# Performance work log

Measured on AMD Instinct MI355X. Metric: run time of the kernel, lower is better.

Reference implementation:

```python
import jax, jax.numpy as jnp
import numpy as np

V = 267735
D_PROJ = 1024
CUTOFF_ENDS = [0, 20000, 40000, 200000, V]   # cutoffs + [vocab]
DIV_VAL = 4
SEQ, BATCH = 64, 8


def setup_inputs() -> dict:
    key = jax.random.key(0)
    ks = jax.random.split(key, 20)
    s = 0.02
    inp = {}
    inp["hidden"] = jax.random.normal(ks[0], (SEQ, BATCH, D_PROJ), dtype=jnp.float32)
    inp["target"] = jax.random.randint(ks[1], (SEQ, BATCH), 0, V)
    n_clusters = len(CUTOFF_ENDS) - 2  # 3
    inp["cluster_weight"] = jax.random.normal(ks[2], (n_clusters, 1024), dtype=jnp.float32) * s
    inp["cluster_bias"] = jnp.zeros((n_clusters,), dtype=jnp.float32)
    k = 3
    for i in range(4):
        l, r = CUTOFF_ENDS[i], CUTOFF_ENDS[i + 1]
        d_i = 1024 // (DIV_VAL ** i)        # 1024, 256, 64, 16
        inp[f"W{i}"] = jax.random.normal(ks[k], (r - l, d_i), dtype=jnp.float32) * s; k += 1
        inp[f"b{i}"] = jnp.zeros((r - l,), dtype=jnp.float32)
        inp[f"proj{i}"] = jax.random.normal(ks[k], (d_i, D_PROJ), dtype=jnp.float32) * s; k += 1
    return inp


def _logit(x, W, b, proj):
    # x: [i,b,d_proj], proj: [d_emb_i, d_proj], W: [n, d_emb_i]
    y = jnp.einsum('ibd,ed->ibe', x, proj)
    return jnp.einsum('ibe,ne->ibn', y, W) + b


def reference(hidden, target, cluster_weight, cluster_bias,
              W0, b0, proj0, W1, b1, proj1, W2, b2, proj2, W3, b3, proj3):
    c0 = CUTOFF_ENDS[1]  # shortlist size (20000)
    # head: shortlist weights concatenated with cluster logits
    head_W = jnp.concatenate([W0, cluster_weight], axis=0)   # [c0 + n_clusters, 1024]
    head_b = jnp.concatenate([b0, cluster_bias], axis=0)
    head_logprob = jax.nn.log_softmax(_logit(hidden, head_W, head_b, proj0), axis=-1)
    out = [head_logprob[..., :c0]]
    tails = [(W1, b1, proj1), (W2, b2, proj2), (W3, b3, proj3)]
    for i, (W, b, proj) in enumerate(tails, start=1):
        tail_logprob = jax.nn.log_softmax(_logit(hidden, W, b, proj), axis=-1)
        # joint logprob = log P(cluster i) + log P(word | cluster i)
        out.append(head_logprob[..., c0 + i - 1, None] + tail_logprob)
    out = jnp.concatenate(out, axis=-1)  # [seq, batch, vocab] of log-probs
    # scatter/gather loss combine is equivalent to gathering the gold log-prob
    gold_lp = jnp.take_along_axis(out, target[..., None], axis=-1)[..., 0]
    loss = -jnp.mean(gold_lp)
    return out, loss
```

## Files before the change

kernel.cpp:

```cpp
#include <hip/hip_runtime.h>

typedef __attribute__((ext_vector_type(8))) short short8;
typedef __attribute__((ext_vector_type(4))) float f32x4;

#define LDC 267735L
#define OUT_ELEMS 137080320L
#define NB_TOT 2094
#define M_FIX 16.0f

__device__ __forceinline__ short f2bf(float f) {
    unsigned u = __float_as_uint(f);
    unsigned r = (u + 0x7fffu + ((u >> 16) & 1u)) >> 16;
    return (short)r;
}
__device__ __forceinline__ float bf2f(short s) {
    return __uint_as_float(((unsigned)(unsigned short)s) << 16);
}
__device__ __forceinline__ short8 cvt8v(f32x4 a, f32x4 b) {
    short8 r;
    r[0] = f2bf(a[0]); r[1] = f2bf(a[1]); r[2] = f2bf(a[2]); r[3] = f2bf(a[3]);
    r[4] = f2bf(b[0]); r[5] = f2bf(b[1]); r[6] = f2bf(b[2]); r[7] = f2bf(b[3]);
    return r;
}

__device__ __forceinline__ void gll16(const short* g, short* l) {
    __builtin_amdgcn_global_load_lds(
        (const __attribute__((address_space(1))) void*)g,
        (__attribute__((address_space(3))) void*)l, 16, 0, 0);
}

__device__ __forceinline__ void conv8(int e, const float* __restrict__ src,
                                      const float* __restrict__ ex, int Nsrc, int Nex,
                                      int Ksrc, int kshift, short* __restrict__ dst)
{
    int r = e >> kshift;
    int c = (e & ((1 << kshift) - 1)) << 3;
    const float* p = nullptr;
    if (r < Nsrc) p = src + (long)r * Ksrc + c;
    else if (r < Nsrc + Nex) p = ex + (long)(r - Nsrc) * Ksrc + c;
    short8 o = {0, 0, 0, 0, 0, 0, 0, 0};
    if (p != nullptr && c < Ksrc) {
        f32x4 a = *(const f32x4*)p;
        f32x4 b = *(const f32x4*)(p + 4);
        o = cvt8v(a, b);
    }
    *(short8*)(dst + (((long)r) << (kshift + 3)) + c) = o;
}

__global__ __launch_bounds__(256) void convert_all(
    const float* __restrict__ W0, const float* __restrict__ cw,
    const float* __restrict__ W1, const float* __restrict__ W2, const float* __restrict__ W3,
    const float* __restrict__ p0, const float* __restrict__ p1,
    const float* __restrict__ p2, const float* __restrict__ p3,
    const float* __restrict__ hidden,
    short* __restrict__ Wb0, short* __restrict__ Wb1,
    short* __restrict__ Wb2, short* __restrict__ Wb3,
    short* __restrict__ pb0, short* __restrict__ pb1,
    short* __restrict__ pb2, short* __restrict__ pb3,
    short* __restrict__ hb)
{
    int b = blockIdx.x;
    int tid = threadIdx.x;
    if (b < 10048)      { conv8((b          ) * 256 + tid, W0, cw, 20000, 3, 1024, 7, Wb0); }
    else if (b < 12560) { conv8((b - 10048  ) * 256 + tid, W1, nullptr, 20000, 0, 256, 5, Wb1); }
    else if (b < 17560) { conv8((b - 12560  ) * 256 + tid, W2, nullptr, 160000, 0, 64, 3, Wb2); }
    else if (b < 18620) { conv8((b - 17560  ) * 256 + tid, W3, nullptr, 67735, 0, 16, 2, Wb3); }
    else if (b < 19132) { conv8((b - 18620  ) * 256 + tid, p0, nullptr, 1024, 0, 1024, 7, pb0); }
    else if (b < 19260) { conv8((b - 19132  ) * 256 + tid, p1, nullptr, 256, 0, 1024, 7, pb1); }
    else if (b < 19324) { conv8((b - 19260  ) * 256 + tid, p2, nullptr, 64, 0, 1024, 7, pb2); }
    else if (b < 19388) { conv8((b - 19324  ) * 256 + tid, p3, nullptr, 16, 0, 1024, 7, pb3); }
    else                { conv8((b - 19388  ) * 256 + tid, hidden, nullptr, 512, 0, 1024, 7, hb); }
}

struct SegP {
    const short* A;
    const short* B;
    const float* bias;
    short* Cb;
    long ldcb;
    int lda, ldb, K, N, Nmain;
};
struct Seg4 { SegP s[4]; };

template<int MODE>
__global__ __launch_bounds__(256, 3) void gemm_uber(
    Seg4 segs, int e0, int e1, int e2,
    const float* __restrict__ cbias, float* __restrict__ clus,
    float* __restrict__ partMS)
{
    __shared__ short As[2][128 * 32];
    __shared__ short Bs[2][128 * 32];
    __shared__ float ps[2][128];

    int bx, ry;
    if (MODE == 1) { bx = blockIdx.x >> 2; ry = blockIdx.x & 3; }
    else           { bx = blockIdx.x;      ry = blockIdx.y; }
    int si = (bx < e0) ? 0 : (bx < e1) ? 1 : (bx < e2) ? 2 : 3;
    int sb = (si == 0) ? 0 : (si == 1) ? e0 : (si == 2) ? e1 : e2;
    const SegP sp = segs.s[si];

    int tid = threadIdx.x;
    int w = tid >> 6, l = tid & 63;
    int wm = w >> 1, wn = w & 1;
    int l15 = l & 15, g = l >> 4, k8 = g << 3;
    int rowBase = ry << 7;
    int colBase = (bx - sb) << 7;

    int sr0 = (w << 5);
    int sr1 = sr0 + 16;
    int lrow = l >> 2;
    int kOff = (l & 3) << 3;
    const short* aG0 = sp.A + (long)(rowBase + sr0 + lrow) * sp.lda + kOff;
    const short* aG1 = sp.A + (long)(rowBase + sr1 + lrow) * sp.lda + kOff;
    const short* bG0 = sp.B + (long)(colBase + sr0 + lrow) * sp.ldb + kOff;
    const short* bG1 = sp.B + (long)(colBase + sr1 + lrow) * sp.ldb + kOff;
    int ldsA0 = sr0 << 5;
    int ldsA1 = sr1 << 5;

    f32x4 acc[4][4];
    #pragma unroll
    for (int i = 0; i < 4; ++i)
        #pragma unroll
        for (int j = 0; j < 4; ++j) acc[i][j] = f32x4{0.f, 0.f, 0.f, 0.f};

    int nt = sp.K >> 5;

    gll16(aG0, &As[0][ldsA0]);
    gll16(aG1, &As[0][ldsA1]);
    gll16(bG0, &Bs[0][ldsA0]);
    gll16(bG1, &Bs[0][ldsA1]);
    __syncthreads();

    int cur = 0;
    #pragma unroll 1
    for (int t = 0; t < nt; ++t) {
        int knext = (t + 1) << 5;
        if (t + 1 < nt) {
            int nb = cur ^ 1;
            gll16(aG0 + knext, &As[nb][ldsA0]);
            gll16(aG1 + knext, &As[nb][ldsA1]);
            gll16(bG0 + knext, &Bs[nb][ldsA0]);
            gll16(bG1 + knext, &Bs[nb][ldsA1]);
        }
        short8 af[4], bf[4];
        #pragma unroll
        for (int mi = 0; mi < 4; ++mi)
            af[mi] = *(const short8*)&As[cur][(((wm << 6) + (mi << 4) + l15) << 5) + k8];
        #pragma unroll
        for (int ni = 0; ni < 4; ++ni)
            bf[ni] = *(const short8*)&Bs[cur][(((wn << 6) + (ni << 4) + l15) << 5) + k8];
        #pragma unroll
        for (int mi = 0; mi < 4; ++mi)
            #pragma unroll
            for (int ni = 0; ni < 4; ++ni)
                acc[mi][ni] = __builtin_amdgcn_mfma_f32_16x16x32_bf16(
                    af[mi], bf[ni], acc[mi][ni], 0, 0, 0);
        __syncthreads();
        cur ^= 1;
    }

    int colv[4];
    float bv4[4];
    #pragma unroll
    for (int ni = 0; ni < 4; ++ni) {
        int col = colBase + (wn << 6) + (ni << 4) + l15;
        colv[ni] = col;
        float bval = 0.f;
        if (MODE == 1) {
            if (col < sp.Nmain) bval = sp.bias[col];
            else if (col < sp.N) bval = cbias[col - sp.Nmain];
        }
        bv4[ni] = bval;
    }

    #pragma unroll
    for (int mi = 0; mi < 4; ++mi) {
        #pragma unroll
        for (int r = 0; r < 4; ++r) {
            int srowg = rowBase + (wm << 6) + (mi << 4) + (g << 2) + r;
            float vals[4];
            #pragma unroll
            for (int ni = 0; ni < 4; ++ni) vals[ni] = acc[mi][ni][r] + bv4[ni];

            if (MODE == 0) {
                #pragma unroll
                for (int ni = 0; ni < 4; ++ni) {
                    int col = colv[ni];
                    if (col < (int)sp.ldcb)
                        sp.Cb[(long)srowg * sp.ldcb + col] = f2bf(vals[ni]);
                }
            } else {
                float s = 0.f;
                #pragma unroll
                for (int ni = 0; ni < 4; ++ni) {
                    int col = colv[ni];
                    if (col < sp.Nmain) {
                        sp.Cb[(long)srowg * sp.ldcb + col] = f2bf(vals[ni]);
                        s += __expf(vals[ni] - M_FIX);
                    } else if (col < sp.N) {
                        clus[srowg * 3 + (col - sp.Nmain)] = vals[ni];
                        s += __expf(vals[ni] - M_FIX);
                    }
                }
                #pragma unroll
                for (int d = 1; d < 16; d <<= 1) s += __shfl_xor(s, d);
                if (l15 == 0) {
                    int rl = (wm << 6) + (mi << 4) + (g << 2) + r;
                    ps[wn][rl] = s;
                }
            }
        }
    }
    if (MODE == 1) {
        __syncthreads();
        if (tid < 128) {
            float S = ps[0][tid] + ps[1][tid];
            partMS[(long)(rowBase + tid) * NB_TOT + bx] = S;
        }
    }
}

__global__ __launch_bounds__(256) void combine_adj(
    const float* __restrict__ partMS, const float* __restrict__ clus,
    float* __restrict__ adjA)
{
    const int segOff[4] = {0, 157, 314, 1564};
    const int segNb[4]  = {157, 157, 1250, 530};
    int row = blockIdx.x, tid = threadIdx.x;
    const float* p = partMS + (long)row * NB_TOT;
    __shared__ float ss[256], Ls[4];
    for (int seg = 0; seg < 4; ++seg) {
        float s = 0.f;
        for (int cb = segOff[seg] + tid; cb < segOff[seg] + segNb[seg]; cb += 256)
            s += p[cb];
        ss[tid] = s;
        __syncthreads();
        for (int off = 128; off > 0; off >>= 1) {
            if (tid < off) ss[tid] += ss[tid + off];
            __syncthreads();
        }
        if (tid == 0) Ls[seg] = logf(ss[0]) + M_FIX;
        __syncthreads();
    }
    if (tid == 0) {
        float l0 = Ls[0];
        adjA[row * 4 + 0] = -l0;
        adjA[row * 4 + 1] = clus[row * 3 + 0] - l0 - Ls[1];
        adjA[row * 4 + 2] = clus[row * 3 + 1] - l0 - Ls[2];
        adjA[row * 4 + 3] = clus[row * 3 + 2] - l0 - Ls[3];
    }
}

__global__ __launch_bounds__(256) void finalize2(
    const short* __restrict__ L0, const short* __restrict__ L1,
    const short* __restrict__ L2, const short* __restrict__ L3,
    const float* __restrict__ adjA, float* __restrict__ out)
{
    int row = blockIdx.y;
    long c0 = ((long)blockIdx.x * 256 + threadIdx.x) * 8;
    if (c0 >= 267735) return;
    const short* src; float adj; long off;
    if (c0 < 20000)       { src = L0 + (long)row * 20000;  off = c0;          adj = adjA[row*4+0]; }
    else if (c0 < 40000)  { src = L1 + (long)row * 20000;  off = c0 - 20000;  adj = adjA[row*4+1]; }
    else if (c0 < 200000) { src = L2 + (long)row * 160000; off = c0 - 40000;  adj = adjA[row*4+2]; }
    else                  { src = L3 + (long)row * 67736;  off = c0 - 200000; adj = adjA[row*4+3]; }
    float* po = out + (long)row * LDC + c0;
    if (c0 + 8 <= 267735) {
        short8 v = *(const short8*)(src + off);
        #pragma unroll
        for (int j = 0; j < 8; ++j) po[j] = bf2f(v[j]) + adj;
    } else {
        for (int j = 0; c0 + j < 267735; ++j) po[j] = bf2f(src[off + j]) + adj;
    }
}

__global__ __launch_bounds__(512) void loss_k(
    const float* __restrict__ out, const int* __restrict__ target,
    float* __restrict__ lossOut)
{
    int tid = threadIdx.x;
    int t = target[tid];
    float v = out[(long)tid * LDC + t];
    __shared__ float sbuf[512];
    sbuf[tid] = v;
    __syncthreads();
    for (int off = 256; off > 0; off >>= 1) {
        if (tid < off) sbuf[tid] += sbuf[tid + off];
        __syncthreads();
    }
    if (tid == 0) lossOut[0] = -sbuf[0] / 512.0f;
}

__device__ __forceinline__ short8 cvt8p(const float* p, bool valid) {
    short8 r = {0, 0, 0, 0, 0, 0, 0, 0};
    if (valid) {
        f32x4 a = *(const f32x4*)p;
        f32x4 b = *(const f32x4*)(p + 4);
        r = cvt8v(a, b);
    }
    return r;
}

#define LDT 40
__global__ __launch_bounds__(256, 2) void gemm_f32(
    const float* __restrict__ A, int lda,
    const float* __restrict__ B, int ldb,
    const float* __restrict__ Wex,
    const float* __restrict__ bias, const float* __restrict__ biasEx,
    float* __restrict__ C, long ldc, long colOffset,
    float* __restrict__ Cex,
    int N, int Nmain, int K)
{
    __shared__ short As[2][128 * LDT];
    __shared__ short Bs[2][128 * LDT];
    int tid = threadIdx.x;
    int w = tid >> 6, l = tid & 63;
    int wm = w >> 1, wn = w & 1;
    int l15 = l & 15, g = l >> 4, k8 = g << 3;
    int rowBase = blockIdx.y << 7;
    int colBase = blockIdx.x << 7;
    int srow = tid >> 1;
    int skc = (tid & 1) << 4;
    const float* aSrc = A + (long)(rowBase + srow) * lda + skc;
    int bn = colBase + srow;
    bool bnv = bn < N;
    const float* bRow = (Wex != nullptr && bn >= Nmain)
                          ? (Wex + (long)(bn - Nmain) * ldb)
                          : (B + (long)(bnv ? bn : 0) * ldb);
    const float* bSrc = bRow + skc;
    int ldsOff = srow * LDT + skc;
    f32x4 acc[4][4];
    #pragma unroll
    for (int i = 0; i < 4; ++i)
        #pragma unroll
        for (int j = 0; j < 4; ++j) acc[i][j] = f32x4{0.f, 0.f, 0.f, 0.f};
    int nt = (K + 31) >> 5;
    {
        bool kv = skc < K;
        *(short8*)&As[0][ldsOff]     = cvt8p(aSrc, kv);
        *(short8*)&As[0][ldsOff + 8] = cvt8p(aSrc + 8, kv);
        *(short8*)&Bs[0][ldsOff]     = cvt8p(bSrc, kv && bnv);
        *(short8*)&Bs[0][ldsOff + 8] = cvt8p(bSrc + 8, kv && bnv);
    }
    __syncthreads();
    int cur = 0;
    #pragma unroll 1
    for (int t = 0; t < nt; ++t) {
        int knext = (t + 1) << 5;
        bool more = knext < K;
        short8 wa0, wa1, wb0, wb1;
        if (more) {
            bool kv = (knext + skc) < K;
            wa0 = cvt8p(aSrc + knext, kv);
            wa1 = cvt8p(aSrc + knext + 8, kv);
            wb0 = cvt8p(bSrc + knext, kv && bnv);
            wb1 = cvt8p(bSrc + knext + 8, kv && bnv);
        }
        short8 af[4], bf[4];
        #pragma unroll
        for (int mi = 0; mi < 4; ++mi)
            af[mi] = *(const short8*)&As[cur][((wm << 6) + (mi << 4) + l15) * LDT + k8];
        #pragma unroll
        for (int ni = 0; ni < 4; ++ni)
            bf[ni] = *(const short8*)&Bs[cur][((wn << 6) + (ni << 4) + l15) * LDT + k8];
        #pragma unroll
        for (int mi = 0; mi < 4; ++mi)
            #pragma unroll
            for (int ni = 0; ni < 4; ++ni)
                acc[mi][ni] = __builtin_amdgcn_mfma_f32_16x16x32_bf16(
                    af[mi], bf[ni], acc[mi][ni], 0, 0, 0);
        if (more) {
            int nb = cur ^ 1;
            *(short8*)&As[nb][ldsOff] = wa0;  *(short8*)&As[nb][ldsOff + 8] = wa1;
            *(short8*)&Bs[nb][ldsOff] = wb0;  *(short8*)&Bs[nb][ldsOff + 8] = wb1;
        }
        __syncthreads();
        cur ^= 1;
    }
    #pragma unroll
    for (int mi = 0; mi < 4; ++mi) {
        #pragma unroll
        for (int r = 0; r < 4; ++r) {
            int srowg = rowBase + (wm << 6) + (mi << 4) + (g << 2) + r;
            #pragma unroll
            for (int ni = 0; ni < 4; ++ni) {
                int col = colBase + (wn << 6) + (ni << 4) + l15;
                float v = acc[mi][ni][r];
                if (col < Nmain) {
                    if (bias) v += bias[col];
                    C[(long)srowg * ldc + colOffset + col] = v;
                } else if (col < N) {
                    if (biasEx) v += biasEx[col - Nmain];
                    Cex[srowg * 3 + (col - Nmain)] = v;
                }
            }
        }
    }
}

__global__ __launch_bounds__(256) void reduce_lse(
    const float* __restrict__ out, const float* __restrict__ clus,
    float* __restrict__ lse)
{
    const int segStart[4] = {0, 20000, 40000, 200000};
    const int segLen[4]   = {20000, 20000, 160000, 67735};
    int seg = blockIdx.x, row = blockIdx.y, tid = threadIdx.x;
    int len = segLen[seg] + (seg == 0 ? 3 : 0);
    const float* p = out + (long)row * LDC + segStart[seg];
    float m = -1e30f, s = 0.f;
    for (int i = tid; i < len; i += 256) {
        float x = (seg == 0 && i >= 20000) ? clus[row * 3 + (i - 20000)] : p[i];
        if (x > m) { s *= __expf(m - x); m = x; }
        s += __expf(x - m);
    }
    __shared__ float sm[256], ss[256];
    sm[tid] = m; ss[tid] = s;
    __syncthreads();
    for (int off = 128; off > 0; off >>= 1) {
        if (tid < off) {
            float m1 = sm[tid], s1 = ss[tid];
            float m2 = sm[tid + off], s2 = ss[tid + off];
            float M = fmaxf(m1, m2);
            sm[tid] = M;
            ss[tid] = s1 * __expf(m1 - M) + s2 * __expf(m2 - M);
        }
        __syncthreads();
    }
    if (tid == 0) lse[row * 4 + seg] = sm[0] + logf(ss[0]);
}

__global__ __launch_bounds__(256) void finalize_k(
    float* __restrict__ out, const float* __restrict__ lse,
    const float* __restrict__ clus)
{
    int row = blockIdx.y;
    long base = (long)row * LDC;
    float l0 = lse[row * 4 + 0];
    float a0 = -l0;
    float a1 = clus[row * 3 + 0] - l0 - lse[row * 4 + 1];
    float a2 = clus[row * 3 + 1] - l0 - lse[row * 4 + 2];
    float a3 = clus[row * 3 + 2] - l0 - lse[row * 4 + 3];
    int v = blockIdx.x * blockDim.x + threadIdx.x;
    int col = v * 4;
    if (col + 4 <= 267735) {
        float adj = col < 20000 ? a0 : col < 40000 ? a1 : col < 200000 ? a2 : a3;
        float* p = out + base + col;
        p[0] += adj; p[1] += adj; p[2] += adj; p[3] += adj;
    } else if (col < 267735) {
        for (int c = col; c < 267735; ++c) out[base + c] += a3;
    }
}

extern "C" void kernel_launch(void* const* d_in, const int* in_sizes, int n_in,
                              void* d_out, int out_size, void* d_ws, size_t ws_size,
                              hipStream_t stream) {
    const float* hidden = (const float*)d_in[0];
    const int*   target = (const int*)d_in[1];
    const float* cw = (const float*)d_in[2];
    const float* cb = (const float*)d_in[3];
    const float* W0 = (const float*)d_in[4];
    const float* b0 = (const float*)d_in[5];
    const float* p0 = (const float*)d_in[6];
    const float* W1 = (const float*)d_in[7];
    const float* b1 = (const float*)d_in[8];
    const float* p1 = (const float*)d_in[9];
    const float* W2 = (const float*)d_in[10];
    const float* b2 = (const float*)d_in[11];
    const float* p2 = (const float*)d_in[12];
    const float* W3 = (const float*)d_in[13];
    const float* b3 = (const float*)d_in[14];
    const float* p3 = (const float*)d_in[15];

    float* out = (float*)d_out;
    dim3 blk(256);

    float* fp = (float*)d_ws;
    float* partMS = fp;
    float* clus = partMS + 1072128;
    float* adjA = clus + 1536;
    short* sb = (short*)(adjA + 2048);
    size_t o = 0;
    short* hb  = sb + o; o += 512 * 1024;
    short* y0b = sb + o; o += 512 * 1024;
    short* y1b = sb + o; o += 512 * 256;
    short* y2b = sb + o; o += 512 * 64;
    short* y3b = sb + o; o += 512 * 32;
    short* pb0 = sb + o; o += 1024 * 1024;
    short* pb1 = sb + o; o += 256 * 1024;
    short* pb2 = sb + o; o += 128 * 1024;
    short* pb3 = sb + o; o += 128 * 1024;
    short* Wb0 = sb + o; o += 20096L * 1024;
    short* Wb1 = sb + o; o += 20096L * 256;
    short* Wb2 = sb + o; o += 160000L * 64;
    short* Wb3 = sb + o; o += 67840L * 32;
    short* L0c = sb + o; o += 512L * 20000;
    short* L1c = sb + o; o += 512L * 20000;
    short* L2c = sb + o; o += 512L * 160000;
    short* L3c = sb + o; o += 512L * 67736;
    size_t needFast = (char*)(sb + o) - (char*)d_ws;

    if (ws_size >= needFast) {
        convert_all<<<dim3(19644), blk, 0, stream>>>(
            W0, cw, W1, W2, W3, p0, p1, p2, p3, hidden,
            Wb0, Wb1, Wb2, Wb3, pb0, pb1, pb2, pb3, hb);

        Seg4 pj;
        pj.s[0] = {hb, pb0, nullptr, y0b, 1024, 1024, 1024, 1024, 1024, 1024};
        pj.s[1] = {hb, pb1, nullptr, y1b, 256,  1024, 1024, 1024, 256,  256};
        pj.s[2] = {hb, pb2, nullptr, y2b, 64,   1024, 1024, 1024, 64,   64};
        pj.s[3] = {hb, pb3, nullptr, y3b, 32,   1024, 1024, 1024, 32,   32};
        gemm_uber<0><<<dim3(12, 4), blk, 0, stream>>>(pj, 8, 10, 11, nullptr, nullptr, nullptr);

        Seg4 lg;
        lg.s[0] = {y0b, Wb0, b0, L0c, 20000,  1024, 1024, 1024, 20003,  20000};
        lg.s[1] = {y1b, Wb1, b1, L1c, 20000,  256,  256,  256,  20000,  20000};
        lg.s[2] = {y2b, Wb2, b2, L2c, 160000, 64,   64,   64,   160000, 160000};
        lg.s[3] = {y3b, Wb3, b3, L3c, 67736,  32,   32,   32,   67735,  67735};
        gemm_uber<1><<<dim3(2094 * 4), blk, 0, stream>>>(lg, 157, 314, 1564, cb, clus, partMS);

        combine_adj<<<dim3(512), blk, 0, stream>>>(partMS, clus, adjA);
        finalize2<<<dim3(131, 512), blk, 0, stream>>>(L0c, L1c, L2c, L3c, adjA, out);
        loss_k<<<dim3(1), dim3(512), 0, stream>>>(out, target, out + OUT_ELEMS);
        return;
    }

    float* ws = (float*)d_ws;
    float* y0 = ws;
    float* y1 = y0 + 512 * 1024;
    float* y2 = y1 + 512 * 256;
    float* y3 = y2 + 512 * 64;
    float* clusF = y3 + 512 * 16;
    float* lseF = clusF + 512 * 3;

    gemm_f32<<<dim3(8, 4), blk, 0, stream>>>(hidden, 1024, p0, 1024, nullptr, nullptr, nullptr,
                                             y0, 1024, 0, nullptr, 1024, 1024, 1024);
    gemm_f32<<<dim3(2, 4), blk, 0, stream>>>(hidden, 1024, p1, 1024, nullptr, nullptr, nullptr,
                                             y1, 256, 0, nullptr, 256, 256, 1024);
    gemm_f32<<<dim3(1, 4), blk, 0, stream>>>(hidden, 1024, p2, 1024, nullptr, nullptr, nullptr,
                                             y2, 64, 0, nullptr, 64, 64, 1024);
    gemm_f32<<<dim3(1, 4), blk, 0, stream>>>(hidden, 1024, p3, 1024, nullptr, nullptr, nullptr,
                                             y3, 16, 0, nullptr, 16, 16, 1024);
    gemm_f32<<<dim3(157, 4), blk, 0, stream>>>(y0, 1024, W0, 1024, cw, b0, cb,
                                               out, LDC, 0, clusF, 20003, 20000, 1024);
    gemm_f32<<<dim3(157, 4), blk, 0, stream>>>(y1, 256, W1, 256, nullptr, b1, nullptr,
                                               out, LDC, 20000, nullptr, 20000, 20000, 256);
    gemm_f32<<<dim3(1250, 4), blk, 0, stream>>>(y2, 64, W2, 64, nullptr, b2, nullptr,
                                                out, LDC, 40000, nullptr, 160000, 160000, 64);
    gemm_f32<<<dim3(530, 4), blk, 0, stream>>>(y3, 16, W3, 16, nullptr, b3, nullptr,
                                               out, LDC, 200000, nullptr, 67735, 67735, 16);
    reduce_lse<<<dim3(4, 512), blk, 0, stream>>>(out, clusF, lseF);
    finalize_k<<<dim3(262, 512), blk, 0, stream>>>(out, lseF, clusF);
    loss_k<<<dim3(1), dim3(512), 0, stream>>>(out, target, out + OUT_ELEMS);
}
```

Measured before the change: 380.5 us.

## Recompute logits GEMM instead of storing bf16 logits intermediates

```diff
diff --git a/kernel.cpp b/kernel.cpp
--- a/kernel.cpp
+++ b/kernel.cpp
@@ -78,6 +78,7 @@
     const float* bias;
     short* Cb;
     long ldcb;
+    long colOff;
     int lda, ldb, K, N, Nmain;
 };
 struct Seg4 { SegP s[4]; };
@@ -86,14 +87,15 @@
 __global__ __launch_bounds__(256, 3) void gemm_uber(
     Seg4 segs, int e0, int e1, int e2,
     const float* __restrict__ cbias, float* __restrict__ clus,
-    float* __restrict__ partMS)
+    float* __restrict__ partMS,
+    float* __restrict__ outF, const float* __restrict__ adjA)
 {
     __shared__ short As[2][128 * 32];
     __shared__ short Bs[2][128 * 32];
     __shared__ float ps[2][128];
 
     int bx, ry;
-    if (MODE == 1) { bx = blockIdx.x >> 2; ry = blockIdx.x & 3; }
+    if (MODE != 0) { bx = blockIdx.x >> 2; ry = blockIdx.x & 3; }
     else           { bx = blockIdx.x;      ry = blockIdx.y; }
     int si = (bx < e0) ? 0 : (bx < e1) ? 1 : (bx < e2) ? 2 : 3;
     int sb = (si == 0) ? 0 : (si == 1) ? e0 : (si == 2) ? e1 : e2;
@@ -166,7 +168,7 @@
         int col = colBase + (wn << 6) + (ni << 4) + l15;
         colv[ni] = col;
         float bval = 0.f;
-        if (MODE == 1) {
+        if (MODE != 0) {
             if (col < sp.Nmain) bval = sp.bias[col];
             else if (col < sp.N) bval = cbias[col - sp.Nmain];
         }
@@ -189,13 +191,20 @@
                     if (col < (int)sp.ldcb)
                         sp.Cb[(long)srowg * sp.ldcb + col] = f2bf(vals[ni]);
                 }
+            } else if (MODE == 2) {
+                float adj = adjA[srowg * 4 + si];
+                float* po = outF + (long)srowg * LDC + sp.colOff;
+                #pragma unroll
+                for (int ni = 0; ni < 4; ++ni) {
+                    int col = colv[ni];
+                    if (col < sp.Nmain) po[col] = vals[ni] + adj;
+                }
             } else {
                 float s = 0.f;
                 #pragma unroll
                 for (int ni = 0; ni < 4; ++ni) {
                     int col = colv[ni];
                     if (col < sp.Nmain) {
-                        sp.Cb[(long)srowg * sp.ldcb + col] = f2bf(vals[ni]);
                         s += __expf(vals[ni] - M_FIX);
                     } else if (col < sp.N) {
                         clus[srowg * 3 + (col - sp.Nmain)] = vals[ni];
@@ -211,7 +220,7 @@
             }
         }
     }
-    if (MODE == 1) {
+    if (MODE == 3) {
         __syncthreads();
         if (tid < 128) {
             float S = ps[0][tid] + ps[1][tid];
@@ -248,29 +257,6 @@
         adjA[row * 4 + 1] = clus[row * 3 + 0] - l0 - Ls[1];
         adjA[row * 4 + 2] = clus[row * 3 + 1] - l0 - Ls[2];
         adjA[row * 4 + 3] = clus[row * 3 + 2] - l0 - Ls[3];
-    }
-}
-
-__global__ __launch_bounds__(256) void finalize2(
-    const short* __restrict__ L0, const short* __restrict__ L1,
-    const short* __restrict__ L2, const short* __restrict__ L3,
-    const float* __restrict__ adjA, float* __restrict__ out)
-{
-    int row = blockIdx.y;
-    long c0 = ((long)blockIdx.x * 256 + threadIdx.x) * 8;
-    if (c0 >= 267735) return;
-    const short* src; float adj; long off;
-    if (c0 < 20000)       { src = L0 + (long)row * 20000;  off = c0;          adj = adjA[row*4+0]; }
-    else if (c0 < 40000)  { src = L1 + (long)row * 20000;  off = c0 - 20000;  adj = adjA[row*4+1]; }
-    else if (c0 < 200000) { src = L2 + (long)row * 160000; off = c0 - 40000;  adj = adjA[row*4+2]; }
-    else                  { src = L3 + (long)row * 67736;  off = c0 - 200000; adj = adjA[row*4+3]; }
-    float* po = out + (long)row * LDC + c0;
-    if (c0 + 8 <= 267735) {
-        short8 v = *(const short8*)(src + off);
-        #pragma unroll
-        for (int j = 0; j < 8; ++j) po[j] = bf2f(v[j]) + adj;
-    } else {
-        for (int j = 0; c0 + j < 267735; ++j) po[j] = bf2f(src[off + j]) + adj;
     }
 }
 
@@ -493,10 +479,6 @@
     short* Wb1 = sb + o; o += 20096L * 256;
     short* Wb2 = sb + o; o += 160000L * 64;
     short* Wb3 = sb + o; o += 67840L * 32;
-    short* L0c = sb + o; o += 512L * 20000;
-    short* L1c = sb + o; o += 512L * 20000;
-    short* L2c = sb + o; o += 512L * 160000;
-    short* L3c = sb + o; o += 512L * 67736;
     size_t needFast = (char*)(sb + o) - (char*)d_ws;
 
     if (ws_size >= needFast) {
@@ -505,21 +487,27 @@
             Wb0, Wb1, Wb2, Wb3, pb0, pb1, pb2, pb3, hb);
 
         Seg4 pj;
-        pj.s[0] = {hb, pb0, nullptr, y0b, 1024, 1024, 1024, 1024, 1024, 1024};
-        pj.s[1] = {hb, pb1, nullptr, y1b, 256,  1024, 1024, 1024, 256,  256};
-        pj.s[2] = {hb, pb2, nullptr, y2b, 64,   1024, 1024, 1024, 64,   64};
-        pj.s[3] = {hb, pb3, nullptr, y3b, 32,   1024, 1024, 1024, 32,   32};
-        gemm_uber<0><<<dim3(12, 4), blk, 0, stream>>>(pj, 8, 10, 11, nullptr, nullptr, nullptr);
+        pj.s[0] = {hb, pb0, nullptr, y0b, 1024, 0, 1024, 1024, 1024, 1024, 1024};
+        pj.s[1] = {hb, pb1, nullptr, y1b, 256,  0, 1024, 1024, 1024, 256,  256};
+        pj.s[2] = {hb, pb2, nullptr, y2b, 64,   0, 1024, 1024, 1024, 64,   64};
+        pj.s[3] = {hb, pb3, nullptr, y3b, 32,   0, 1024, 1024, 1024, 32,   32};
+        gemm_uber<0><<<dim3(12, 4), blk, 0, stream>>>(
+            pj, 8, 10, 11, nullptr, nullptr, nullptr, nullptr, nullptr);
 
         Seg4 lg;
-        lg.s[0] = {y0b, Wb0, b0, L0c, 20000,  1024, 1024, 1024, 20003,  20000};
-        lg.s[1] = {y1b, Wb1, b1, L1c, 20000,  256,  256,  256,  20000,  20000};
-        lg.s[2] = {y2b, Wb2, b2, L2c, 160000, 64,   64,   64,   160000, 160000};
-        lg.s[3] = {y3b, Wb3, b3, L3c, 67736,  32,   32,   32,   67735,  67735};
-        gemm_uber<1><<<dim3(2094 * 4), blk, 0, stream>>>(lg, 157, 314, 1564, cb, clus, partMS);
+        lg.s[0] = {y0b, Wb0, b0, nullptr, 0, 0,      1024, 1024, 1024, 20003,  20000};
+        lg.s[1] = {y1b, Wb1, b1, nullptr, 0, 20000,  256,  256,  256,  20000,  20000};
+        lg.s[2] = {y2b, Wb2, b2, nullptr, 0, 40000,  64,   64,   64,   160000, 160000};
+        lg.s[3] = {y3b, Wb3, b3, nullptr, 0, 200000, 32,   32,   32,   67735,  67735};
+
+        gemm_uber<3><<<dim3(2094 * 4), blk, 0, stream>>>(
+            lg, 157, 314, 1564, cb, clus, partMS, nullptr, nullptr);
 
         combine_adj<<<dim3(512), blk, 0, stream>>>(partMS, clus, adjA);
-        finalize2<<<dim3(131, 512), blk, 0, stream>>>(L0c, L1c, L2c, L3c, adjA, out);
+
+        gemm_uber<2><<<dim3(2094 * 4), blk, 0, stream>>>(
+            lg, 157, 314, 1564, cb, nullptr, nullptr, out, adjA);
+
         loss_k<<<dim3(1), dim3(512), 0, stream>>>(out, target, out + OUT_ELEMS);
         return;
     }
```

After: 388.2 us. +2.0%, slower.
